# Optimization experiments

Hardware: AMD Instinct MI355X
Metric: run time of the kernel (lower is better)

## Reference

```python
import jax, jax.numpy as jnp
import numpy as np

HIDDEN = 3584
H = 28          # num attention heads
KV = 4          # num key-value heads
HD = 128        # head dim
MROPE = [16, 24, 24]  # sum*2 == HD
EPS = 1e-6
S_TOT = 4096
N_SAMPLES = 4


def rmsnorm(x, w, eps=EPS):
    return x * jax.lax.rsqrt(jnp.mean(x * x, axis=-1, keepdims=True) + eps) * w


def rotate_half(x):
    x1, x2 = jnp.split(x, 2, axis=-1)
    return jnp.concatenate([-x2, x1], axis=-1)


def mrope_merge(t):
    # t: [3, S, HD] -> [S, HD], section i taken from rope axis i%3
    cuts = np.cumsum(np.array(MROPE) * 2)[:-1]
    parts = jnp.split(t, cuts, axis=-1)
    return jnp.concatenate([p[i % 3] for i, p in enumerate(parts)], axis=-1)


def setup_inputs() -> dict:
    key = jax.random.key(0)
    ks = iter(jax.random.split(key, 32))
    std = 0.02

    def w(shape):
        return jax.random.normal(next(ks), shape, dtype=jnp.float32) * std

    inp = {
        "packed_sequence": jax.random.normal(next(ks), (S_TOT, HIDDEN), dtype=jnp.float32),
        "packed_cos": jax.random.uniform(next(ks), (3, S_TOT, HD), dtype=jnp.float32, minval=-1.0, maxval=1.0),
        "packed_sin": jax.random.uniform(next(ks), (3, S_TOT, HD), dtype=jnp.float32, minval=-1.0, maxval=1.0),
    }
    # und / geo indices partition [0, S_TOT)
    inp["packed_und_token_indexes"] = jnp.arange(S_TOT // 2, dtype=jnp.int64 if jax.config.jax_enable_x64 else jnp.int32)
    inp["packed_geo_token_indexes"] = jnp.arange(S_TOT // 2, dtype=inp["packed_und_token_indexes"].dtype) + S_TOT // 2
    inp["sample_len"] = S_TOT // N_SAMPLES

    for tag in ("und", "geo"):
        inp[f"q_w_{tag}"] = w((H * HD, HIDDEN))
        inp[f"q_b_{tag}"] = jnp.zeros((H * HD,), jnp.float32)
        inp[f"k_w_{tag}"] = w((KV * HD, HIDDEN))
        inp[f"k_b_{tag}"] = jnp.zeros((KV * HD,), jnp.float32)
        inp[f"v_w_{tag}"] = w((KV * HD, HIDDEN))
        inp[f"v_b_{tag}"] = jnp.zeros((KV * HD,), jnp.float32)
        inp[f"o_w_{tag}"] = w((HIDDEN, H * HD))
        inp[f"q_norm_{tag}"] = jnp.ones((HD,), jnp.float32)
        inp[f"k_norm_{tag}"] = jnp.ones((HD,), jnp.float32)
    return inp


def reference(packed_sequence, packed_cos, packed_sin,
              q_w_und, q_b_und, k_w_und, k_b_und, v_w_und, v_b_und, o_w_und,
              q_norm_und, k_norm_und,
              q_w_geo, q_b_geo, k_w_geo, k_b_geo, v_w_geo, v_b_geo, o_w_geo,
              q_norm_geo, k_norm_geo,
              packed_und_token_indexes, packed_geo_token_indexes, sample_len):
    S, D = packed_sequence.shape
    G = H // KV
    und, geo = packed_und_token_indexes, packed_geo_token_indexes
    xu = packed_sequence[und]
    xg = packed_sequence[geo]

    def scatter(dim, fu, fg):
        out = jnp.zeros((S, dim), packed_sequence.dtype)
        return out.at[und].set(fu).at[geo].set(fg)

    # modality-routed QKV projections (gather -> gemm -> scatter)
    q = scatter(H * HD, xu @ q_w_und.T + q_b_und, xg @ q_w_geo.T + q_b_geo).reshape(S, H, HD)
    k = scatter(KV * HD, xu @ k_w_und.T + k_b_und, xg @ k_w_geo.T + k_b_geo).reshape(S, KV, HD)
    v = scatter(KV * HD, xu @ v_w_und.T + v_b_und, xg @ v_w_geo.T + v_b_geo).reshape(S, KV, HD)

    # per-modality QK RMSNorm
    qn = jnp.zeros_like(q).at[und].set(rmsnorm(q[und], q_norm_und)).at[geo].set(rmsnorm(q[geo], q_norm_geo))
    kn = jnp.zeros_like(k).at[und].set(rmsnorm(k[und], k_norm_und)).at[geo].set(rmsnorm(k[geo], k_norm_geo))

    # multimodal rotary embedding
    cos = mrope_merge(packed_cos)[:, None, :]  # [S,1,HD]
    sin = mrope_merge(packed_sin)[:, None, :]
    qr = qn * cos + rotate_half(qn) * sin
    kr = kn * cos + rotate_half(kn) * sin

    # block-diagonal causal attention over packed equal-length samples
    L = int(sample_len)
    B = S // L
    qb = qr.reshape(B, L, H, HD)
    kb = jnp.repeat(kr.reshape(B, L, KV, HD), G, axis=2)  # GQA expansion
    vb = jnp.repeat(v.reshape(B, L, KV, HD), G, axis=2)
    scores = jnp.einsum('blhd,bmhd->bhlm', qb, kb) / np.sqrt(HD).astype(np.float32)
    causal = jnp.tril(jnp.ones((L, L), bool))
    scores = jnp.where(causal, scores, jnp.finfo(scores.dtype).min)
    attn = jax.nn.softmax(scores, axis=-1)
    out = jnp.einsum('bhlm,bmhd->blhd', attn, vb).reshape(S, H * HD)

    # modality-routed output projection
    res = jnp.zeros((S, D), packed_sequence.dtype)
    res = res.at[und].set(out[und] @ o_w_und.T).at[geo].set(out[geo] @ o_w_geo.T)
    return res
```

## Files before the change

kernel.cpp:

```cpp
#include <hip/hip_runtime.h>
#include <hip/hip_bf16.h>
#include <stdint.h>

#define HIDDEN 3584
#define NH 28
#define NKV 4
#define HD 128
#define GQ (NH / NKV)
#define NQKV ((NH + 2 * NKV) * HD)
#define LSAMP 1024

typedef __bf16 bf16x8 __attribute__((ext_vector_type(8)));
typedef float f32x4 __attribute__((ext_vector_type(4)));

__device__ __forceinline__ unsigned short f2bf(float f) {
  unsigned int u = __float_as_uint(f);
  u += 0x7fffu + ((u >> 16) & 1u);
  return (unsigned short)(u >> 16);
}
__device__ __forceinline__ float bf2f(unsigned short h) {
  return __uint_as_float(((unsigned int)h) << 16);
}

__device__ __forceinline__ void gload16(const void* g, void* l) {
  __builtin_amdgcn_global_load_lds(
      (const __attribute__((address_space(1))) void*)g,
      (__attribute__((address_space(3))) void*)l, 16, 0, 0);
}

__global__ void build_maps_kernel(const int* __restrict__ und, const int* __restrict__ geo,
                                  int nu, int ng,
                                  int* __restrict__ row_of_token, int* __restrict__ tok_of_row,
                                  int* __restrict__ mod_of_token) {
  int i = blockIdx.x * 256 + threadIdx.x;
  if (i < nu) {
    int t = und[i];
    row_of_token[t] = i; tok_of_row[i] = t; mod_of_token[t] = 0;
  } else if (i < nu + ng) {
    int j = i - nu;
    int t = geo[j];
    row_of_token[t] = nu + j; tok_of_row[nu + j] = t; mod_of_token[t] = 1;
  }
}

struct Cvt8 {
  const float* src[8];
  unsigned short* dst[8];
  int cum[8];
};
__global__ void convert8_kernel(Cvt8 a, int tot4) {
  int i = blockIdx.x * blockDim.x + threadIdx.x;
  const int stride = gridDim.x * blockDim.x;
  for (; i < tot4; i += stride) {
    int seg = 0;
#pragma unroll
    for (int s2 = 1; s2 < 8; ++s2) seg += (i >= a.cum[s2]);
    const int off = i - a.cum[seg];
    float4 v = reinterpret_cast<const float4*>(a.src[seg])[off];
    reinterpret_cast<ushort4*>(a.dst[seg])[off] =
        make_ushort4(f2bf(v.x), f2bf(v.y), f2bf(v.z), f2bf(v.w));
  }
}

__global__ void gather_x_kernel(const float* __restrict__ X, const int* __restrict__ tok_of_row,
                                unsigned short* __restrict__ Xg) {
  const int r = blockIdx.x;
  const int tok = tok_of_row[r];
  const float4* src = reinterpret_cast<const float4*>(X + (size_t)tok * HIDDEN);
  ushort4* dst = reinterpret_cast<ushort4*>(Xg + (size_t)r * HIDDEN);
  for (int i = threadIdx.x; i < HIDDEN / 4; i += 256) {
    float4 v = src[i];
    dst[i] = make_ushort4(f2bf(v.x), f2bf(v.y), f2bf(v.z), f2bf(v.w));
  }
}

template <int OUTMODE, int NT, int WR, int WC, int NF>
__global__ __launch_bounds__(NT, (NT / 64 + 3) / 4)
void gemm2_kernel(const unsigned short* __restrict__ A,
                  const unsigned short* __restrict__ W0, const unsigned short* __restrict__ W1,
                  const float* __restrict__ qb0, const float* __restrict__ kb0, const float* __restrict__ vb0,
                  const float* __restrict__ qb1, const float* __restrict__ kb1, const float* __restrict__ vb1,
                  unsigned short* __restrict__ Obf, float* __restrict__ Of32,
                  const int* __restrict__ tok_of_row,
                  int nu, int ng, int N, int K, int NX, int NY) {
  constexpr int MF = 256 / WR / 16;
  constexpr int BN = WC * NF * 16;
  constexpr int BUFSZ = 32768 + BN * 128;
  constexpr int ACH = 2048;
  constexpr int BCH = BN * 8;
  __shared__ char lds[2 * BUFSZ];

  const int nwg = NX * NY * 2;
  int id = blockIdx.x + NX * (blockIdx.y + NY * blockIdx.z);
  {
    const int q = nwg >> 3, r = nwg & 7;
    const int xcd = id & 7, pos = id >> 3;
    id = (xcd < r ? xcd * (q + 1) : r * (q + 1) + (xcd - r) * q) + pos;
  }
  const int bx = id % NX;
  const int byz = id / NX;
  const int by = byz % NY;
  const int bz = byz / NY;

  const int baseRow = bz ? nu : 0;
  const int Mcount = bz ? ng : nu;
  const int mbase = by * 256;
  if (mbase >= Mcount) return;
  const unsigned short* W = bz ? W1 : W0;

  const int t = threadIdx.x;
  const int w = t >> 6, l = t & 63;
  const int l15 = l & 15, l4 = l >> 4;
  const int wr = w / WC, wc = w % WC;
  const int wrr = wr * (MF * 16), wcc = wc * (NF * 16);
  const int ncol0 = bx * BN;
  const int krev = w & 1;

  f32x4 acc[MF][NF] = {};

  const int nk = K >> 6;

  auto stage = [&](int bufIdx, int kt) {
    char* base = lds + bufIdx * BUFSZ;
    const int k0 = kt * 64;
#pragma unroll
    for (int c0 = 0; c0 < ACH; c0 += NT) {
      const int c = c0 + t;
      if (c < ACH) {
        const int row = c >> 3, slot = c & 7;
        const int srck = (slot ^ (row & 7)) << 3;
        int ar = mbase + row; if (ar >= Mcount) ar = Mcount - 1;
        gload16(A + (size_t)(baseRow + ar) * K + k0 + srck, base + c * 16);
      }
    }
#pragma unroll
    for (int c0 = 0; c0 < BCH; c0 += NT) {
      const int c = c0 + t;
      if (c < BCH) {
        const int row = c >> 3, slot = c & 7;
        const int srck = (slot ^ (row & 7)) << 3;
        gload16(W + (size_t)(ncol0 + row) * K + k0 + srck, base + 32768 + c * 16);
      }
    }
  };

  stage(0, 0);
  asm volatile("s_waitcnt vmcnt(0)\n\ts_barrier" ::: "memory");

  for (int kt = 0; kt < nk; ++kt) {
    char* Ab = lds + (kt & 1) * BUFSZ;
    char* Bb = Ab + 32768;

    if (kt + 1 < nk) stage((kt + 1) & 1, kt + 1);
    __builtin_amdgcn_sched_barrier(0);

#pragma unroll
    for (int ks = 0; ks < 2; ++ks) {
      const int kss = krev ? (1 - ks) : ks;
      bf16x8 af[MF], bfr[NF];
#pragma unroll
      for (int mf = 0; mf < MF; ++mf) {
        const int row = wrr + mf * 16 + l15;
        af[mf] = *reinterpret_cast<const bf16x8*>(Ab + row * 128 + (((kss * 4 + l4) ^ (row & 7)) << 4));
      }
#pragma unroll
      for (int nf = 0; nf < NF; ++nf) {
        const int row = wcc + nf * 16 + l15;
        bfr[nf] = *reinterpret_cast<const bf16x8*>(Bb + row * 128 + (((kss * 4 + l4) ^ (row & 7)) << 4));
      }
      __builtin_amdgcn_s_setprio(1);
#pragma unroll
      for (int mf = 0; mf < MF; ++mf)
#pragma unroll
        for (int nf = 0; nf < NF; ++nf)
          acc[mf][nf] = __builtin_amdgcn_mfma_f32_16x16x32_bf16(af[mf], bfr[nf], acc[mf][nf], 0, 0, 0);
      __builtin_amdgcn_s_setprio(0);
    }

    if (kt + 1 < nk) {
      asm volatile("s_waitcnt vmcnt(0)\n\ts_barrier" ::: "memory");
    }
  }

#pragma unroll
  for (int mf = 0; mf < MF; ++mf) {
#pragma unroll
    for (int rr = 0; rr < 4; ++rr) {
      const int ml = mbase + wrr + mf * 16 + l4 * 4 + rr;
      if (ml >= Mcount) continue;
      int trow = 0;
      if (OUTMODE == 1) trow = tok_of_row[baseRow + ml];
#pragma unroll
      for (int nf = 0; nf < NF; ++nf) {
        const int n = ncol0 + wcc + nf * 16 + l15;
        const float v = acc[mf][nf][rr];
        if (OUTMODE == 0) {
          const float* qb = bz ? qb1 : qb0;
          const float* kb = bz ? kb1 : kb0;
          const float* vb = bz ? vb1 : vb0;
          const float bias = (n < NH * HD) ? qb[n]
                              : ((n < (NH + NKV) * HD) ? kb[n - NH * HD] : vb[n - (NH + NKV) * HD]);
          Obf[(size_t)(baseRow + ml) * N + n] = f2bf(v + bias);
        } else {
          Of32[(size_t)trow * N + n] = v;
        }
      }
    }
  }
}

__global__ __launch_bounds__(64)
void norm_rope_kernel(const unsigned short* __restrict__ Y,
                      const int* __restrict__ row_of_token, const int* __restrict__ mod_of_token,
                      const float* __restrict__ pcos, const float* __restrict__ psin,
                      const float* __restrict__ qn_u, const float* __restrict__ kn_u,
                      const float* __restrict__ qn_g, const float* __restrict__ kn_g,
                      unsigned short* __restrict__ Qr,
                      unsigned short* __restrict__ Kr,
                      unsigned short* __restrict__ Vt,
                      int S) {
  const int s = blockIdx.x, t = threadIdx.x;
  const int r = row_of_token[s];
  const int m = mod_of_token[s];
  const float* qn = m ? qn_g : qn_u;
  const float* kn = m ? kn_g : kn_u;
  const int d0 = t, d1 = t + 64;
  const int a0 = (d0 < 32) ? 0 : (d0 < 80 ? 1 : 2);
  const int a1 = (d1 < 80) ? 1 : 2;
  const float c0 = pcos[((size_t)a0 * S + s) * HD + d0];
  const float c1 = pcos[((size_t)a1 * S + s) * HD + d1];
  const float s0 = psin[((size_t)a0 * S + s) * HD + d0];
  const float s1 = psin[((size_t)a1 * S + s) * HD + d1];
  const float qnw0 = qn[t], qnw1 = qn[t + 64];
  const float knw0 = kn[t], knw1 = kn[t + 64];
  const unsigned short* yrow = Y + (size_t)r * NQKV;
  constexpr float SC = 0.08838834764831845f;

#pragma unroll 4
  for (int hh = 0; hh < NH; ++hh) {
    float x0 = bf2f(yrow[hh * HD + t]);
    float x1 = bf2f(yrow[hh * HD + t + 64]);
    float ss = x0 * x0 + x1 * x1;
#pragma unroll
    for (int dd = 1; dd < 64; dd <<= 1) ss += __shfl_xor(ss, dd);
    const float rs = rsqrtf(ss * (1.f / 128.f) + 1e-6f);
    const float q0 = x0 * rs * qnw0, q1 = x1 * rs * qnw1;
    unsigned short* dst = Qr + ((size_t)hh * S + s) * HD;
    dst[t] = f2bf((q0 * c0 - q1 * s0) * SC);
    dst[t + 64] = f2bf((q1 * c1 + q0 * s1) * SC);
  }
#pragma unroll
  for (int kh = 0; kh < NKV; ++kh) {
    float x0 = bf2f(yrow[NH * HD + kh * HD + t]);
    float x1 = bf2f(yrow[NH * HD + kh * HD + t + 64]);
    float ss = x0 * x0 + x1 * x1;
#pragma unroll
    for (int dd = 1; dd < 64; dd <<= 1) ss += __shfl_xor(ss, dd);
    const float rs = rsqrtf(ss * (1.f / 128.f) + 1e-6f);
    const float k0 = x0 * rs * knw0, k1 = x1 * rs * knw1;
    unsigned short* dst = Kr + ((size_t)kh * S + s) * HD;
    dst[t] = f2bf(k0 * c0 - k1 * s0);
    dst[t + 64] = f2bf(k1 * c1 + k0 * s1);
  }
#pragma unroll
  for (int vh = 0; vh < NKV; ++vh) {
    float x0 = bf2f(yrow[(NH + NKV) * HD + vh * HD + t]);
    float x1 = bf2f(yrow[(NH + NKV) * HD + vh * HD + t + 64]);
    Vt[((size_t)(vh * HD + t)) * S + s] = f2bf(x0);
    Vt[((size_t)(vh * HD + t + 64)) * S + s] = f2bf(x1);
  }
}

__global__ __launch_bounds__(256, 2)
void attn_kernel(const unsigned short* __restrict__ Qr, const unsigned short* __restrict__ Kr,
                 const unsigned short* __restrict__ Vt, const int* __restrict__ row_of_token,
                 unsigned short* __restrict__ Og, int S, int NXQ) {
  __shared__ char lds[2 * 16384 + 2 * 16384 + 64 * 144];
  char* Plds = lds + 65536;
  const int h = blockIdx.y, b = blockIdx.z;
  const int kvh = h / GQ;
  const int t = threadIdx.x, w = t >> 6, l = t & 63;
  const int l15 = l & 15, l4 = l >> 4;
  const int sbase = b * LSAMP;

  auto stage = [&](int bufIdx, int kt) {
    char* Kb = lds + bufIdx * 16384;
    char* Vb = lds + 32768 + bufIdx * 16384;
    const int kb0 = sbase + kt * 64;
#pragma unroll
    for (int i = 0; i < 4; ++i) {
      const int c = t + i * 256;
      const int row = c >> 4, slot = c & 15;
      const int srcs = slot ^ (row & 15);
      gload16(Kr + ((size_t)kvh * S + kb0 + row) * HD + srcs * 8, Kb + c * 16);
    }
#pragma unroll
    for (int i = 0; i < 4; ++i) {
      const int c = t + i * 256;
      const int row = c >> 3, slot = c & 7;
      const int srcs = slot ^ (row & 7);
      gload16(Vt + (size_t)(kvh * HD + row) * S + kb0 + srcs * 8, Vb + c * 16);
    }
  };

  for (int pass = 0; pass < 2; ++pass) {
    const int qt = pass ? (NXQ - 1 - blockIdx.x) : blockIdx.x;

    bf16x8 aq[4];
    {
      const int qrow = sbase + qt * 64 + w * 16 + l15;
      const unsigned short* qp = Qr + ((size_t)h * S + qrow) * HD + l4 * 8;
#pragma unroll
      for (int kk = 0; kk < 4; ++kk) aq[kk] = *reinterpret_cast<const bf16x8*>(qp + kk * 32);
    }
    f32x4 acc[8] = {};
    float mr[4] = {-INFINITY, -INFINITY, -INFINITY, -INFINITY};
    float lr[4] = {0.f, 0.f, 0.f, 0.f};

    stage(0, 0);
    asm volatile("s_waitcnt vmcnt(0)\n\ts_barrier" ::: "memory");

    for (int kt = 0; kt <= qt; ++kt) {
      char* Kb = lds + (kt & 1) * 16384;
      char* Vb = lds + 32768 + (kt & 1) * 16384;

      if (kt < qt) stage((kt + 1) & 1, kt + 1);
      __builtin_amdgcn_sched_barrier(0);

      f32x4 sa[4] = {};
#pragma unroll
      for (int kk = 0; kk < 4; ++kk) {
        bf16x8 bk[4];
#pragma unroll
        for (int nf = 0; nf < 4; ++nf) {
          const int row = nf * 16 + l15;
          const int slot = kk * 4 + l4;
          bk[nf] = *reinterpret_cast<const bf16x8*>(Kb + row * 256 + ((slot ^ (row & 15)) << 4));
        }
#pragma unroll
        for (int nf = 0; nf < 4; ++nf)
          sa[nf] = __builtin_amdgcn_mfma_f32_16x16x32_bf16(aq[kk], bk[nf], sa[nf], 0, 0, 0);
      }

      const int qg = qt * 64 + w * 16 + l4 * 4;
#pragma unroll
      for (int nf = 0; nf < 4; ++nf) {
        const int cg = kt * 64 + nf * 16 + l15;
#pragma unroll
        for (int rr = 0; rr < 4; ++rr)
          if (cg > qg + rr) sa[nf][rr] = -INFINITY;
      }

      float pv[4][4];
#pragma unroll
      for (int rr = 0; rr < 4; ++rr) {
        float mx = fmaxf(fmaxf(sa[0][rr], sa[1][rr]), fmaxf(sa[2][rr], sa[3][rr]));
        mx = fmaxf(mx, mr[rr]);
#pragma unroll
        for (int dd = 1; dd < 16; dd <<= 1) mx = fmaxf(mx, __shfl_xor(mx, dd));
        const float alpha = __expf(mr[rr] - mx);
        mr[rr] = mx;
        float part = 0.f;
#pragma unroll
        for (int nf = 0; nf < 4; ++nf) {
          const float p = __expf(sa[nf][rr] - mx);
          pv[nf][rr] = p;
          part += p;
        }
        lr[rr] = lr[rr] * alpha + part;
#pragma unroll
        for (int nf2 = 0; nf2 < 8; ++nf2) acc[nf2][rr] *= alpha;
      }

#pragma unroll
      for (int rr = 0; rr < 4; ++rr) {
        const int row = w * 16 + l4 * 4 + rr;
#pragma unroll
        for (int nf = 0; nf < 4; ++nf)
          ((unsigned short*)(Plds + row * 144))[nf * 16 + l15] = f2bf(pv[nf][rr]);
      }

#pragma unroll
      for (int kk2 = 0; kk2 < 2; ++kk2) {
        const bf16x8 ap = *reinterpret_cast<const bf16x8*>(Plds + (w * 16 + l15) * 144 + kk2 * 64 + l4 * 16);
#pragma unroll
        for (int nf2 = 0; nf2 < 8; ++nf2) {
          const int rowd = nf2 * 16 + l15;
          const int slot = kk2 * 4 + l4;
          const bf16x8 bv = *reinterpret_cast<const bf16x8*>(Vb + rowd * 128 + ((slot ^ (rowd & 7)) << 4));
          acc[nf2] = __builtin_amdgcn_mfma_f32_16x16x32_bf16(ap, bv, acc[nf2], 0, 0, 0);
        }
      }

      if (kt < qt) {
        asm volatile("s_waitcnt vmcnt(0)\n\ts_barrier" ::: "memory");
      }
    }

#pragma unroll
    for (int rr = 0; rr < 4; ++rr)
#pragma unroll
      for (int dd = 1; dd < 16; dd <<= 1) lr[rr] += __shfl_xor(lr[rr], dd);

    const int srow0 = sbase + qt * 64 + w * 16 + l4 * 4;
#pragma unroll
    for (int rr = 0; rr < 4; ++rr) {
      const float inv = 1.f / lr[rr];
      const int mrow = row_of_token[srow0 + rr];
      unsigned short* orow = Og + (size_t)mrow * (NH * HD) + h * HD;
#pragma unroll
      for (int nf2 = 0; nf2 < 8; ++nf2) orow[nf2 * 16 + l15] = f2bf(acc[nf2][rr] * inv);
    }

    if (pass == 0) {
      asm volatile("s_waitcnt vmcnt(0) lgkmcnt(0)\n\ts_barrier" ::: "memory");
    }
  }
}

extern "C" void kernel_launch(void* const* d_in, const int* in_sizes, int n_in,
                              void* d_out, int out_size, void* d_ws, size_t ws_size,
                              hipStream_t stream) {
  const float* X = (const float*)d_in[0];
  const float* pcos = (const float*)d_in[1];
  const float* psin = (const float*)d_in[2];
  const int* und = (const int*)d_in[3];
  const int* geo = (const int*)d_in[4];
  const int nu = in_sizes[3], ng = in_sizes[4];
  const int S = in_sizes[0] / HIDDEN;

  const float* qw[2] = {(const float*)d_in[6], (const float*)d_in[15]};
  const float* qb[2] = {(const float*)d_in[7], (const float*)d_in[16]};
  const float* kw[2] = {(const float*)d_in[8], (const float*)d_in[17]};
  const float* kb[2] = {(const float*)d_in[9], (const float*)d_in[18]};
  const float* vw[2] = {(const float*)d_in[10], (const float*)d_in[19]};
  const float* vb[2] = {(const float*)d_in[11], (const float*)d_in[20]};
  const float* ow[2] = {(const float*)d_in[12], (const float*)d_in[21]};
  const float* qn[2] = {(const float*)d_in[13], (const float*)d_in[22]};
  const float* kn[2] = {(const float*)d_in[14], (const float*)d_in[23]};

  char* ws = (char*)d_ws;
  size_t off = 0;
  auto alloc = [&](size_t bytes) {
    char* p = ws + off;
    off = (off + bytes + 255) & ~(size_t)255;
    return p;
  };
  int* row_of_token = (int*)alloc((size_t)S * 4);
  int* tok_of_row = (int*)alloc((size_t)S * 4);
  int* mod_of_token = (int*)alloc((size_t)S * 4);
  unsigned short* Wqkv[2] = {(unsigned short*)alloc((size_t)NQKV * HIDDEN * 2),
                             (unsigned short*)alloc((size_t)NQKV * HIDDEN * 2)};
  unsigned short* Wo[2] = {(unsigned short*)alloc((size_t)HIDDEN * HIDDEN * 2),
                           (unsigned short*)alloc((size_t)HIDDEN * HIDDEN * 2)};
  unsigned short* Xg = (unsigned short*)alloc((size_t)S * HIDDEN * 2);
  unsigned short* Yqkv = (unsigned short*)alloc((size_t)S * NQKV * 2);
  unsigned short* Qr = (unsigned short*)alloc((size_t)NH * S * HD * 2);
  unsigned short* Kr = (unsigned short*)alloc((size_t)NKV * S * HD * 2);
  unsigned short* Vt = (unsigned short*)alloc((size_t)NKV * S * HD * 2);
  unsigned short* Og = (unsigned short*)alloc((size_t)S * NH * HD * 2);
  (void)ws_size; (void)n_in; (void)out_size;

  build_maps_kernel<<<(S + 255) / 256, 256, 0, stream>>>(und, geo, nu, ng,
                                                         row_of_token, tok_of_row, mod_of_token);
  {
    Cvt8 ca;
    const float* srcs[8] = {qw[0], kw[0], vw[0], ow[0], qw[1], kw[1], vw[1], ow[1]};
    unsigned short* dsts[8] = {
        Wqkv[0], Wqkv[0] + (size_t)NH * HD * HIDDEN, Wqkv[0] + (size_t)(NH + NKV) * HD * HIDDEN, Wo[0],
        Wqkv[1], Wqkv[1] + (size_t)NH * HD * HIDDEN, Wqkv[1] + (size_t)(NH + NKV) * HD * HIDDEN, Wo[1]};
    const int n4s[8] = {NH * HD * HIDDEN / 4, NKV * HD * HIDDEN / 4, NKV * HD * HIDDEN / 4, HIDDEN * HIDDEN / 4,
                        NH * HD * HIDDEN / 4, NKV * HD * HIDDEN / 4, NKV * HD * HIDDEN / 4, HIDDEN * HIDDEN / 4};
    int cum = 0;
    for (int i = 0; i < 8; ++i) { ca.src[i] = srcs[i]; ca.dst[i] = dsts[i]; ca.cum[i] = cum; cum += n4s[i]; }
    convert8_kernel<<<2048, 256, 0, stream>>>(ca, cum);
  }
  gather_x_kernel<<<S, 256, 0, stream>>>(X, tok_of_row, Xg);

  const int maxM = (nu > ng ? nu : ng);
  {
    const int NX = NQKV / 288, NY = (maxM + 255) / 256;
    gemm2_kernel<0, 768, 4, 3, 6><<<dim3(NX, NY, 2), 768, 0, stream>>>(
        Xg, Wqkv[0], Wqkv[1], qb[0], kb[0], vb[0], qb[1], kb[1], vb[1],
        Yqkv, nullptr, nullptr, nu, ng, NQKV, HIDDEN, NX, NY);
  }

  norm_rope_kernel<<<S, 64, 0, stream>>>(Yqkv, row_of_token, mod_of_token, pcos, psin,
                                         qn[0], kn[0], qn[1], kn[1], Qr, Kr, Vt, S);

  {
    const int NXQ = LSAMP / 64;
    attn_kernel<<<dim3(NXQ / 2, NH, S / LSAMP), 256, 0, stream>>>(Qr, Kr, Vt, row_of_token, Og, S, NXQ);
  }

  {
    const int NX = HIDDEN / 224, NY = (maxM + 255) / 256;
    gemm2_kernel<1, 512, 4, 2, 7><<<dim3(NX, NY, 2), 512, 0, stream>>>(
        Og, Wo[0], Wo[1], nullptr, nullptr, nullptr, nullptr, nullptr, nullptr,
        nullptr, (float*)d_out, tok_of_row, nu, ng, HIDDEN, HIDDEN, NX, NY);
  }
}
```

Before: 408.6 us.

## Share K/V tiles across GQA heads in attention and vectorize norm-rope

The attention kernel now launches one 448-thread block per KV head, with each of the 7 waves handling one query head of the group. A single LDS-staged K/V tile is shared by all 7 heads instead of being reloaded per head, and each wave processes two 16-row query fragments over a 32-row query tile. The norm/rope kernel is rewritten so each thread loads 8 contiguous bf16 values, a 16-lane shuffle does the reduction, and rotate_half uses a shuffle. The aim is to cut redundant K/V global traffic and improve vector width, at the cost of more registers per wave (one block per CU by launch bounds) and a causal tile granularity of 64 keys against 32 queries.

After: 392.6 us. -3.9%, faster.

```diff
diff --git a/kernel.cpp b/kernel.cpp
--- a/kernel.cpp
+++ b/kernel.cpp
@@ -219,84 +219,105 @@
                       unsigned short* __restrict__ Kr,
                       unsigned short* __restrict__ Vt,
                       int S) {
-  const int s = blockIdx.x, t = threadIdx.x;
+  const int s = blockIdx.x, l = threadIdx.x;
+  const int g = l >> 4, l15 = l & 15;
+  const int d0 = l15 * 8;
+  const int axis = (d0 < 32) ? 0 : (d0 < 80 ? 1 : 2);
   const int r = row_of_token[s];
   const int m = mod_of_token[s];
   const float* qn = m ? qn_g : qn_u;
   const float* kn = m ? kn_g : kn_u;
-  const int d0 = t, d1 = t + 64;
-  const int a0 = (d0 < 32) ? 0 : (d0 < 80 ? 1 : 2);
-  const int a1 = (d1 < 80) ? 1 : 2;
-  const float c0 = pcos[((size_t)a0 * S + s) * HD + d0];
-  const float c1 = pcos[((size_t)a1 * S + s) * HD + d1];
-  const float s0 = psin[((size_t)a0 * S + s) * HD + d0];
-  const float s1 = psin[((size_t)a1 * S + s) * HD + d1];
-  const float qnw0 = qn[t], qnw1 = qn[t + 64];
-  const float knw0 = kn[t], knw1 = kn[t + 64];
+  const bool hi = l15 >= 8;
+  const float rsign = hi ? 1.f : -1.f;
+  constexpr float SC = 0.08838834764831845f;
+
+  float c8[8], s8[8], qw8[8], kw8[8];
+  {
+    const float* cp = pcos + ((size_t)axis * S + s) * HD + d0;
+    const float* sp = psin + ((size_t)axis * S + s) * HD + d0;
+#pragma unroll
+    for (int j = 0; j < 8; ++j) { c8[j] = cp[j]; s8[j] = sp[j]; }
+#pragma unroll
+    for (int j = 0; j < 8; ++j) { qw8[j] = qn[d0 + j]; kw8[j] = kn[d0 + j]; }
+  }
   const unsigned short* yrow = Y + (size_t)r * NQKV;
-  constexpr float SC = 0.08838834764831845f;
-
-#pragma unroll 4
-  for (int hh = 0; hh < NH; ++hh) {
-    float x0 = bf2f(yrow[hh * HD + t]);
-    float x1 = bf2f(yrow[hh * HD + t + 64]);
-    float ss = x0 * x0 + x1 * x1;
-#pragma unroll
-    for (int dd = 1; dd < 64; dd <<= 1) ss += __shfl_xor(ss, dd);
+
+#pragma unroll
+  for (int grp = 0; grp < 7; ++grp) {
+    const int hh = grp * 4 + g;
+    const bf16x8 y = *reinterpret_cast<const bf16x8*>(yrow + hh * HD + d0);
+    float x[8], xw[8];
+    float ss = 0.f;
+#pragma unroll
+    for (int j = 0; j < 8; ++j) { x[j] = bf2f(((unsigned short*)&y)[j]); ss += x[j] * x[j]; }
+#pragma unroll
+    for (int dd = 1; dd < 16; dd <<= 1) ss += __shfl_xor(ss, dd);
+    const float rs = rsqrtf(ss * (1.f / 128.f) + 1e-6f) * SC;
+#pragma unroll
+    for (int j = 0; j < 8; ++j) xw[j] = x[j] * qw8[j];
+    unsigned short o[8];
+#pragma unroll
+    for (int j = 0; j < 8; ++j) {
+      const float xp = __shfl_xor(xw[j], 8);
+      o[j] = f2bf(rs * (xw[j] * c8[j] + rsign * xp * s8[j]));
+    }
+    *reinterpret_cast<ushort4*>(Qr + ((size_t)hh * S + s) * HD + d0) = make_ushort4(o[0], o[1], o[2], o[3]);
+    *reinterpret_cast<ushort4*>(Qr + ((size_t)hh * S + s) * HD + d0 + 4) = make_ushort4(o[4], o[5], o[6], o[7]);
+  }
+
+  {
+    const int kh = g;
+    const bf16x8 y = *reinterpret_cast<const bf16x8*>(yrow + (NH + kh) * HD + d0);
+    float x[8], xw[8];
+    float ss = 0.f;
+#pragma unroll
+    for (int j = 0; j < 8; ++j) { x[j] = bf2f(((unsigned short*)&y)[j]); ss += x[j] * x[j]; }
+#pragma unroll
+    for (int dd = 1; dd < 16; dd <<= 1) ss += __shfl_xor(ss, dd);
     const float rs = rsqrtf(ss * (1.f / 128.f) + 1e-6f);
-    const float q0 = x0 * rs * qnw0, q1 = x1 * rs * qnw1;
-    unsigned short* dst = Qr + ((size_t)hh * S + s) * HD;
-    dst[t] = f2bf((q0 * c0 - q1 * s0) * SC);
-    dst[t + 64] = f2bf((q1 * c1 + q0 * s1) * SC);
-  }
-#pragma unroll
-  for (int kh = 0; kh < NKV; ++kh) {
-    float x0 = bf2f(yrow[NH * HD + kh * HD + t]);
-    float x1 = bf2f(yrow[NH * HD + kh * HD + t + 64]);
-    float ss = x0 * x0 + x1 * x1;
-#pragma unroll
-    for (int dd = 1; dd < 64; dd <<= 1) ss += __shfl_xor(ss, dd);
-    const float rs = rsqrtf(ss * (1.f / 128.f) + 1e-6f);
-    const float k0 = x0 * rs * knw0, k1 = x1 * rs * knw1;
-    unsigned short* dst = Kr + ((size_t)kh * S + s) * HD;
-    dst[t] = f2bf(k0 * c0 - k1 * s0);
-    dst[t + 64] = f2bf(k1 * c1 + k0 * s1);
-  }
-#pragma unroll
-  for (int vh = 0; vh < NKV; ++vh) {
-    float x0 = bf2f(yrow[(NH + NKV) * HD + vh * HD + t]);
-    float x1 = bf2f(yrow[(NH + NKV) * HD + vh * HD + t + 64]);
-    Vt[((size_t)(vh * HD + t)) * S + s] = f2bf(x0);
-    Vt[((size_t)(vh * HD + t + 64)) * S + s] = f2bf(x1);
-  }
-}
-
-__global__ __launch_bounds__(256, 2)
-void attn_kernel(const unsigned short* __restrict__ Qr, const unsigned short* __restrict__ Kr,
-                 const unsigned short* __restrict__ Vt, const int* __restrict__ row_of_token,
-                 unsigned short* __restrict__ Og, int S, int NXQ) {
-  __shared__ char lds[2 * 16384 + 2 * 16384 + 64 * 144];
-  char* Plds = lds + 65536;
-  const int h = blockIdx.y, b = blockIdx.z;
-  const int kvh = h / GQ;
+#pragma unroll
+    for (int j = 0; j < 8; ++j) xw[j] = x[j] * kw8[j];
+    unsigned short o[8];
+#pragma unroll
+    for (int j = 0; j < 8; ++j) {
+      const float xp = __shfl_xor(xw[j], 8);
+      o[j] = f2bf(rs * (xw[j] * c8[j] + rsign * xp * s8[j]));
+    }
+    *reinterpret_cast<ushort4*>(Kr + ((size_t)kh * S + s) * HD + d0) = make_ushort4(o[0], o[1], o[2], o[3]);
+    *reinterpret_cast<ushort4*>(Kr + ((size_t)kh * S + s) * HD + d0 + 4) = make_ushort4(o[4], o[5], o[6], o[7]);
+  }
+
+  {
+    const int vh = g;
+    const bf16x8 y = *reinterpret_cast<const bf16x8*>(yrow + (NH + NKV + vh) * HD + d0);
+#pragma unroll
+    for (int j = 0; j < 8; ++j)
+      Vt[((size_t)(vh * HD + d0 + j)) * S + s] = ((unsigned short*)&y)[j];
+  }
+}
+
+__global__ __launch_bounds__(448, 1)
+void attn7_kernel(const unsigned short* __restrict__ Qr, const unsigned short* __restrict__ Kr,
+                  const unsigned short* __restrict__ Vt, const int* __restrict__ row_of_token,
+                  unsigned short* __restrict__ Og, int S) {
+  __shared__ char lds[2 * 16384 + 2 * 16384 + 7 * 4608];
+  const int kvh = blockIdx.y, b = blockIdx.z;
   const int t = threadIdx.x, w = t >> 6, l = t & 63;
   const int l15 = l & 15, l4 = l >> 4;
+  const int h = kvh * GQ + w;
   const int sbase = b * LSAMP;
+  char* Plds = lds + 65536 + w * 4608;
 
   auto stage = [&](int bufIdx, int kt) {
     char* Kb = lds + bufIdx * 16384;
     char* Vb = lds + 32768 + bufIdx * 16384;
     const int kb0 = sbase + kt * 64;
-#pragma unroll
-    for (int i = 0; i < 4; ++i) {
-      const int c = t + i * 256;
+    for (int c = t; c < 1024; c += 448) {
       const int row = c >> 4, slot = c & 15;
       const int srcs = slot ^ (row & 15);
       gload16(Kr + ((size_t)kvh * S + kb0 + row) * HD + srcs * 8, Kb + c * 16);
     }
-#pragma unroll
-    for (int i = 0; i < 4; ++i) {
-      const int c = t + i * 256;
+    for (int c = t; c < 1024; c += 448) {
       const int row = c >> 3, slot = c & 7;
       const int srcs = slot ^ (row & 7);
       gload16(Vt + (size_t)(kvh * HD + row) * S + kb0 + srcs * 8, Vb + c * 16);
@@ -304,30 +325,35 @@
   };
 
   for (int pass = 0; pass < 2; ++pass) {
-    const int qt = pass ? (NXQ - 1 - blockIdx.x) : blockIdx.x;
-
-    bf16x8 aq[4];
-    {
-      const int qrow = sbase + qt * 64 + w * 16 + l15;
+    const int q32 = pass ? (31 - blockIdx.x) : blockIdx.x;
+    const int nkt = q32 / 2 + 1;
+
+    bf16x8 aq[2][4];
+#pragma unroll
+    for (int fr = 0; fr < 2; ++fr) {
+      const int qrow = sbase + q32 * 32 + fr * 16 + l15;
       const unsigned short* qp = Qr + ((size_t)h * S + qrow) * HD + l4 * 8;
 #pragma unroll
-      for (int kk = 0; kk < 4; ++kk) aq[kk] = *reinterpret_cast<const bf16x8*>(qp + kk * 32);
-    }
-    f32x4 acc[8] = {};
-    float mr[4] = {-INFINITY, -INFINITY, -INFINITY, -INFINITY};
-    float lr[4] = {0.f, 0.f, 0.f, 0.f};
+      for (int kk = 0; kk < 4; ++kk) aq[fr][kk] = *reinterpret_cast<const bf16x8*>(qp + kk * 32);
+    }
+    f32x4 acc[2][8] = {};
+    float mr[2][4], lr[2][4];
+#pragma unroll
+    for (int fr = 0; fr < 2; ++fr)
+#pragma unroll
+      for (int rr = 0; rr < 4; ++rr) { mr[fr][rr] = -INFINITY; lr[fr][rr] = 0.f; }
 
     stage(0, 0);
     asm volatile("s_waitcnt vmcnt(0)\n\ts_barrier" ::: "memory");
 
-    for (int kt = 0; kt <= qt; ++kt) {
+    for (int kt = 0; kt < nkt; ++kt) {
       char* Kb = lds + (kt & 1) * 16384;
       char* Vb = lds + 32768 + (kt & 1) * 16384;
 
-      if (kt < qt) stage((kt + 1) & 1, kt + 1);
+      if (kt + 1 < nkt) stage((kt + 1) & 1, kt + 1);
       __builtin_amdgcn_sched_barrier(0);
 
-      f32x4 sa[4] = {};
+      f32x4 sa[2][4] = {};
 #pragma unroll
       for (int kk = 0; kk < 4; ++kk) {
         bf16x8 bk[4];
@@ -338,78 +364,85 @@
           bk[nf] = *reinterpret_cast<const bf16x8*>(Kb + row * 256 + ((slot ^ (row & 15)) << 4));
         }
 #pragma unroll
-        for (int nf = 0; nf < 4; ++nf)
-          sa[nf] = __builtin_amdgcn_mfma_f32_16x16x32_bf16(aq[kk], bk[nf], sa[nf], 0, 0, 0);
-      }
-
-      const int qg = qt * 64 + w * 16 + l4 * 4;
-#pragma unroll
-      for (int nf = 0; nf < 4; ++nf) {
-        const int cg = kt * 64 + nf * 16 + l15;
-#pragma unroll
-        for (int rr = 0; rr < 4; ++rr)
-          if (cg > qg + rr) sa[nf][rr] = -INFINITY;
-      }
-
-      float pv[4][4];
-#pragma unroll
-      for (int rr = 0; rr < 4; ++rr) {
-        float mx = fmaxf(fmaxf(sa[0][rr], sa[1][rr]), fmaxf(sa[2][rr], sa[3][rr]));
-        mx = fmaxf(mx, mr[rr]);
-#pragma unroll
-        for (int dd = 1; dd < 16; dd <<= 1) mx = fmaxf(mx, __shfl_xor(mx, dd));
-        const float alpha = __expf(mr[rr] - mx);
-        mr[rr] = mx;
-        float part = 0.f;
+        for (int fr = 0; fr < 2; ++fr)
+#pragma unroll
+          for (int nf = 0; nf < 4; ++nf)
+            sa[fr][nf] = __builtin_amdgcn_mfma_f32_16x16x32_bf16(aq[fr][kk], bk[nf], sa[fr][nf], 0, 0, 0);
+      }
+
+#pragma unroll
+      for (int fr = 0; fr < 2; ++fr) {
+        const int qg = q32 * 32 + fr * 16 + l4 * 4;
 #pragma unroll
         for (int nf = 0; nf < 4; ++nf) {
-          const float p = __expf(sa[nf][rr] - mx);
-          pv[nf][rr] = p;
-          part += p;
+          const int cg = kt * 64 + nf * 16 + l15;
+#pragma unroll
+          for (int rr = 0; rr < 4; ++rr)
+            if (cg > qg + rr) sa[fr][nf][rr] = -INFINITY;
         }
-        lr[rr] = lr[rr] * alpha + part;
-#pragma unroll
-        for (int nf2 = 0; nf2 < 8; ++nf2) acc[nf2][rr] *= alpha;
-      }
-
-#pragma unroll
-      for (int rr = 0; rr < 4; ++rr) {
-        const int row = w * 16 + l4 * 4 + rr;
-#pragma unroll
-        for (int nf = 0; nf < 4; ++nf)
-          ((unsigned short*)(Plds + row * 144))[nf * 16 + l15] = f2bf(pv[nf][rr]);
+#pragma unroll
+        for (int rr = 0; rr < 4; ++rr) {
+          float mx = fmaxf(fmaxf(sa[fr][0][rr], sa[fr][1][rr]), fmaxf(sa[fr][2][rr], sa[fr][3][rr]));
+          mx = fmaxf(mx, mr[fr][rr]);
+#pragma unroll
+          for (int dd = 1; dd < 16; dd <<= 1) mx = fmaxf(mx, __shfl_xor(mx, dd));
+          const float alpha = __expf(mr[fr][rr] - mx);
+          mr[fr][rr] = mx;
+          float part = 0.f;
+#pragma unroll
+          for (int nf = 0; nf < 4; ++nf) {
+            const float p = __expf(sa[fr][nf][rr] - mx);
+            sa[fr][nf][rr] = p;
+            part += p;
+          }
+          lr[fr][rr] = lr[fr][rr] * alpha + part;
+#pragma unroll
+          for (int nf2 = 0; nf2 < 8; ++nf2) acc[fr][nf2][rr] *= alpha;
+        }
+#pragma unroll
+        for (int rr = 0; rr < 4; ++rr) {
+          const int row = fr * 16 + l4 * 4 + rr;
+#pragma unroll
+          for (int nf = 0; nf < 4; ++nf)
+            ((unsigned short*)(Plds + row * 144))[nf * 16 + l15] = f2bf(sa[fr][nf][rr]);
+        }
       }
 
 #pragma unroll
       for (int kk2 = 0; kk2 < 2; ++kk2) {
-        const bf16x8 ap = *reinterpret_cast<const bf16x8*>(Plds + (w * 16 + l15) * 144 + kk2 * 64 + l4 * 16);
+        bf16x8 ap[2];
+#pragma unroll
+        for (int fr = 0; fr < 2; ++fr)
+          ap[fr] = *reinterpret_cast<const bf16x8*>(Plds + (fr * 16 + l15) * 144 + kk2 * 64 + l4 * 16);
 #pragma unroll
         for (int nf2 = 0; nf2 < 8; ++nf2) {
           const int rowd = nf2 * 16 + l15;
           const int slot = kk2 * 4 + l4;
           const bf16x8 bv = *reinterpret_cast<const bf16x8*>(Vb + rowd * 128 + ((slot ^ (rowd & 7)) << 4));
-          acc[nf2] = __builtin_amdgcn_mfma_f32_16x16x32_bf16(ap, bv, acc[nf2], 0, 0, 0);
+#pragma unroll
+          for (int fr = 0; fr < 2; ++fr)
+            acc[fr][nf2] = __builtin_amdgcn_mfma_f32_16x16x32_bf16(ap[fr], bv, acc[fr][nf2], 0, 0, 0);
         }
       }
 
-      if (kt < qt) {
+      if (kt + 1 < nkt) {
         asm volatile("s_waitcnt vmcnt(0)\n\ts_barrier" ::: "memory");
       }
     }
 
 #pragma unroll
-    for (int rr = 0; rr < 4; ++rr)
-#pragma unroll
-      for (int dd = 1; dd < 16; dd <<= 1) lr[rr] += __shfl_xor(lr[rr], dd);
-
-    const int srow0 = sbase + qt * 64 + w * 16 + l4 * 4;
-#pragma unroll
-    for (int rr = 0; rr < 4; ++rr) {
-      const float inv = 1.f / lr[rr];
-      const int mrow = row_of_token[srow0 + rr];
-      unsigned short* orow = Og + (size_t)mrow * (NH * HD) + h * HD;
-#pragma unroll
-      for (int nf2 = 0; nf2 < 8; ++nf2) orow[nf2 * 16 + l15] = f2bf(acc[nf2][rr] * inv);
+    for (int fr = 0; fr < 2; ++fr) {
+#pragma unroll
+      for (int rr = 0; rr < 4; ++rr) {
+#pragma unroll
+        for (int dd = 1; dd < 16; dd <<= 1) lr[fr][rr] += __shfl_xor(lr[fr][rr], dd);
+        const float inv = 1.f / lr[fr][rr];
+        const int srow = sbase + q32 * 32 + fr * 16 + l4 * 4 + rr;
+        const int mrow = row_of_token[srow];
+        unsigned short* orow = Og + (size_t)mrow * (NH * HD) + h * HD;
+#pragma unroll
+        for (int nf2 = 0; nf2 < 8; ++nf2) orow[nf2 * 16 + l15] = f2bf(acc[fr][nf2][rr] * inv);
+      }
     }
 
     if (pass == 0) {
@@ -488,10 +521,7 @@
   norm_rope_kernel<<<S, 64, 0, stream>>>(Yqkv, row_of_token, mod_of_token, pcos, psin,
                                          qn[0], kn[0], qn[1], kn[1], Qr, Kr, Vt, S);
 
-  {
-    const int NXQ = LSAMP / 64;
-    attn_kernel<<<dim3(NXQ / 2, NH, S / LSAMP), 256, 0, stream>>>(Qr, Kr, Vt, row_of_token, Og, S, NXQ);
-  }
+  attn7_kernel<<<dim3(16, NKV, S / LSAMP), 448, 0, stream>>>(Qr, Kr, Vt, row_of_token, Og, S);
 
   {
     const int NX = HIDDEN / 224, NY = (maxM + 255) / 256;
```
